# Optimization experiments

Measured on AMD Instinct MI355X. Metric: run time of the kernel, lower is better.

The kernel has to match this reference:

```python
import jax, jax.numpy as jnp
import numpy as np

SCALE = 100.0
ALPHA_MEM = 0.9
ALPHA_P = 0.99
ALPHA_MEM_OUT = 0.9

@jax.custom_vjp
def spike(x):
    return (x > 0).astype(x.dtype)

def _spike_fwd(x):
    return spike(x), x

def _spike_bwd(x, g):
    return (g / (SCALE * jnp.abs(x) + 1.0) ** 2,)

spike.defvjp(_spike_fwd, _spike_bwd)

B, T, N_IN, N, N_OUT = 64, 200, 128, 2048, 20

def setup_inputs() -> dict:
    key = jax.random.key(0)
    ks = jax.random.split(key, 6)
    inputs = jax.random.normal(ks[0], (B, T, N_IN), dtype=jnp.float32)
    w = jax.random.normal(ks[1], (N, N), dtype=jnp.float32) / np.sqrt(N)
    wscale_in = 1.0 - ALPHA_MEM
    w_in = jax.random.normal(ks[2], (N_IN, N), dtype=jnp.float32) * (wscale_in / np.sqrt(N_IN))
    wscale_out = 1.0 - ALPHA_MEM_OUT
    w_out = jax.random.normal(ks[3], (N, N_OUT), dtype=jnp.float32) * (wscale_out / np.sqrt(N))
    w_signs = jnp.sign(jax.random.normal(ks[4], (N,), dtype=jnp.float32))
    p = 0.1 * jax.random.normal(ks[5], (N,), dtype=jnp.float32)
    return {"inputs": inputs, "w": w, "w_in": w_in, "w_out": w_out,
            "w_signs": w_signs, "p": p}

def reference(inputs, w, w_in, w_out, w_signs, p):
    dt = inputs.dtype
    h1 = jnp.einsum('btc,cn->btn', inputs, w_in)          # [B,T,N]
    rec_w = w_signs[:, None] * jnp.abs(w)                  # [N,N]
    depr = (p < 0).astype(dt)                              # [N]

    def step(carry, h1_t):
        mem, w_p = carry
        mthr = mem - 1.0
        out = spike(mthr)
        rst = jax.lax.stop_gradient((mthr > 0).astype(dt))
        syn_p = jnp.einsum('bn,no->bo', out * (1.0 + w_p), rec_w)
        w_p_new = w_p * ALPHA_P + out * p * (1.0 + depr * w_p)
        mem_new = ALPHA_MEM * mem + h1_t + syn_p - rst
        return (mem_new, w_p_new), out

    zeros = jnp.zeros((h1.shape[0], rec_w.shape[0]), dtype=dt)
    _, spk = jax.lax.scan(step, (zeros, zeros), jnp.swapaxes(h1, 0, 1))
    spk_rec = jnp.swapaxes(spk, 0, 1)                      # [B,T,N]

    h2 = jnp.einsum('btn,no->bto', spk_rec, w_out)         # [B,T,O]

    def out_step(o, h2_t):
        o2 = ALPHA_MEM_OUT * o + h2_t
        return o2, o2

    o0 = jnp.zeros((h2.shape[0], h2.shape[2]), dtype=dt)
    _, outs = jax.lax.scan(out_step, o0, jnp.swapaxes(h2, 0, 1))
    return jnp.swapaxes(outs, 0, 1)                        # [B,T,O]
```

## Files before the change

kernel.cpp:

```cpp
#include <hip/hip_runtime.h>

#define BB   64
#define TT   200
#define NIN  128
#define NN   2048
#define NOUT 20

#define S    8
#define NWIN 25
#define ACAP 64
#define BCAP 128

typedef __attribute__((ext_vector_type(8))) short short8;
typedef __attribute__((ext_vector_type(4))) float f32x4;
typedef __attribute__((ext_vector_type(4))) _Float16 h16x4;

__device__ __forceinline__ void bf16split(float x, ushort& h, ushort& l) {
    unsigned u = __float_as_uint(x);
    unsigned hb = (u + 0x7FFFu + ((u >> 16) & 1u)) >> 16;
    h = (ushort)hb;
    float xh = __uint_as_float(hb << 16);
    float xl = x - xh;
    unsigned v = __float_as_uint(xl);
    l = (ushort)((v + 0x7FFFu + ((v >> 16) & 1u)) >> 16);
}

__global__ __launch_bounds__(256) void repack_a(
    const float* __restrict__ X, ushort* __restrict__ Ap)
{
    const int blk  = blockIdx.x;
    const int tid  = threadIdx.x;
    const int kc   = tid >> 6;
    const int lane = tid & 63;
    const int lr   = lane & 15, lg = lane >> 4;

    const float* src = X + (size_t)(blk * 16 + lr) * NIN + kc * 32 + lg * 8;
    float f[8];
    *(float4*)(f)     = *(const float4*)(src);
    *(float4*)(f + 4) = *(const float4*)(src + 4);

    short8 hv, lv;
    #pragma unroll
    for (int j = 0; j < 8; ++j) {
        ushort h, l;
        bf16split(f[j], h, l);
        hv[j] = (short)h; lv[j] = (short)l;
    }
    ushort* dst = Ap + (size_t)(blk * 4 + kc) * 1024 + lane * 8;
    *(short8*)(dst)       = hv;
    *(short8*)(dst + 512) = lv;
}

__global__ __launch_bounds__(256) void repack_b(
    const float* __restrict__ W, ushort* __restrict__ Bp)
{
    const int blk  = blockIdx.x;
    const int tid  = threadIdx.x;
    const int kc   = tid >> 6;
    const int lane = tid & 63;
    const int lr   = lane & 15, lg = lane >> 4;

    const float* src = W + (size_t)(kc * 32 + lg * 8) * NN + blk * 16 + lr;
    float f[8];
    #pragma unroll
    for (int j = 0; j < 8; ++j) f[j] = src[(size_t)j * NN];

    short8 hv, lv;
    #pragma unroll
    for (int j = 0; j < 8; ++j) {
        ushort h, l;
        bf16split(f[j], h, l);
        hv[j] = (short)h; lv[j] = (short)l;
    }
    ushort* dst = Bp + (size_t)(blk * 4 + kc) * 1024 + lane * 8;
    *(short8*)(dst)       = hv;
    *(short8*)(dst + 512) = lv;
}

__global__ __launch_bounds__(256, 2) void h1_mfma(
    const ushort* __restrict__ Ap, const ushort* __restrict__ Bp,
    _Float16* __restrict__ C)
{
    __shared__ ushort sbuf[2][16][1024];

    const int l   = blockIdx.y * gridDim.x + blockIdx.x;
    const int nl  = (l & 7) * 200 + (l >> 3);
    const int bx  = nl & 15, by = nl >> 4;

    const int tid  = threadIdx.x;
    const int w_   = tid >> 6, lane = tid & 63;
    const int lr   = lane & 15, lg = lane >> 4;
    const int m0   = by * 128, n0 = bx * 128;
    const int wr   = (w_ >> 1) * 64, wc = (w_ & 1) * 64;

    const ushort* pAs = Ap + (size_t)(m0 >> 4) * 4096;
    const ushort* pBs = Bp + (size_t)(n0 >> 4) * 4096;

#define STAGE(kc, nb)                                                        \
    do {                                                                     \
        _Pragma("unroll")                                                    \
        for (int i_ = 0; i_ < 8; ++i_) {                                     \
            const int idx_   = w_ * 8 + i_;                                  \
            const int side_  = idx_ >> 4;                                    \
            const int chunk_ = (idx_ >> 1) & 7;                              \
            const int hl_    = idx_ & 1;                                     \
            const ushort* g_ = (side_ ? pBs : pAs) + chunk_ * 4096           \
                               + (kc) * 1024 + hl_ * 512 + lane * 8;         \
            ushort* d_ = &sbuf[nb][idx_ >> 1][hl_ * 512];                    \
            __builtin_amdgcn_global_load_lds(                                \
                (const __attribute__((address_space(1))) void*)g_,           \
                (__attribute__((address_space(3))) void*)d_, 16, 0, 0);      \
        }                                                                    \
    } while (0)

    f32x4 acc[4][4];
    const f32x4 z = {0.f, 0.f, 0.f, 0.f};
    #pragma unroll
    for (int rb = 0; rb < 4; ++rb)
        #pragma unroll
        for (int cb = 0; cb < 4; ++cb) acc[rb][cb] = z;

    STAGE(0, 0);
    __syncthreads();

    const int ar = wr >> 4;
    const int br = 8 + (wc >> 4);

    #pragma unroll
    for (int kc = 0; kc < 4; ++kc) {
        const int cb_ = kc & 1;
        if (kc < 3) STAGE(kc + 1, cb_ ^ 1);

        short8 fah[4], fal[4], fbh[4], fbl[4];
        #pragma unroll
        for (int rb = 0; rb < 4; ++rb) {
            fah[rb] = *(const short8*)(&sbuf[cb_][ar + rb][lane * 8]);
            fal[rb] = *(const short8*)(&sbuf[cb_][ar + rb][512 + lane * 8]);
        }
        #pragma unroll
        for (int cb = 0; cb < 4; ++cb) {
            fbh[cb] = *(const short8*)(&sbuf[cb_][br + cb][lane * 8]);
            fbl[cb] = *(const short8*)(&sbuf[cb_][br + cb][512 + lane * 8]);
        }
        #pragma unroll
        for (int rb = 0; rb < 4; ++rb)
            #pragma unroll
            for (int cb = 0; cb < 4; ++cb) {
                acc[rb][cb] = __builtin_amdgcn_mfma_f32_16x16x32_bf16(
                    fbh[cb], fah[rb], acc[rb][cb], 0, 0, 0);
                acc[rb][cb] = __builtin_amdgcn_mfma_f32_16x16x32_bf16(
                    fbl[cb], fah[rb], acc[rb][cb], 0, 0, 0);
                acc[rb][cb] = __builtin_amdgcn_mfma_f32_16x16x32_bf16(
                    fbh[cb], fal[rb], acc[rb][cb], 0, 0, 0);
            }
        if (kc < 3) __syncthreads();
    }
#undef STAGE

    #pragma unroll
    for (int rb = 0; rb < 4; ++rb) {
        _Float16* Crow = C + (size_t)(m0 + wr + rb * 16 + lr) * NN
                           + n0 + wc + lg * 4;
        #pragma unroll
        for (int cb = 0; cb < 4; ++cb) {
            h16x4 hv;
            hv[0] = (_Float16)acc[rb][cb][0];
            hv[1] = (_Float16)acc[rb][cb][1];
            hv[2] = (_Float16)acc[rb][cb][2];
            hv[3] = (_Float16)acc[rb][cb][3];
            *(h16x4*)(Crow + cb * 16) = hv;
        }
    }
}

__global__ __launch_bounds__(512) void snn_scan(
    const _Float16* __restrict__ h1, const float* __restrict__ w,
    const float* __restrict__ w_signs, const float* __restrict__ pvec,
    const float* __restrict__ w_out, float* __restrict__ out)
{
    const int b   = blockIdx.x;
    const int tid = threadIdx.x;
    const int n0  = tid << 2;

    __shared__ int   s_amask[2];
    __shared__ int   s_acnt[2][S];
    __shared__ int   s_aidx[2][S][ACAP];
    __shared__ float s_aval[2][S][ACAP];
    __shared__ int   s_bcnt[2];
    __shared__ int   s_bidx[2][BCAP];
    __shared__ float s_bval[2][BCAP];

    if (tid < 2) { s_amask[tid] = 0; s_bcnt[tid] = 0; }
    if (tid < 2 * S) ((int*)s_acnt)[tid] = 0;

    float4 mem = {0.f,0.f,0.f,0.f}, wp = {0.f,0.f,0.f,0.f};
    const float4 p4 = *(const float4*)(pvec + n0);
    const float4 sg = *(const float4*)(w_signs + n0);
    float4 depr;
    depr.x = (p4.x < 0.f) ? 1.f : 0.f;  depr.y = (p4.y < 0.f) ? 1.f : 0.f;
    depr.z = (p4.z < 0.f) ? 1.f : 0.f;  depr.w = (p4.w < 0.f) ? 1.f : 0.f;

    const float P99[S] = {1.0f, 0.99f, 0.9801f, 0.970299f, 0.96059601f,
                          0.9509900499f, 0.941480149401f, 0.93206534790699f};
    const float P99_8 = 0.9227446944279201f;

    const _Float16* hb = h1 + (size_t)b * TT * NN + n0;
    float* outb = out + (size_t)b * TT * NOUT + tid;
    float o2 = 0.f;

    h16x4 PA[S], PB[S];
    #pragma unroll
    for (int j = 0; j < S; ++j) PA[j] = *(const h16x4*)(hb + (size_t)j * NN);
    __syncthreads();

#define RAWBAR()                                              \
    do { asm volatile("s_waitcnt lgkmcnt(0)" ::: "memory");   \
         __builtin_amdgcn_s_barrier();                        \
         asm volatile("" ::: "memory"); } while (0)

#define CVT4(v) { (float)(v)[0], (float)(v)[1], (float)(v)[2], (float)(v)[3] }

    auto window = [&](h16x4 (&Pc)[S], h16x4 (&Pf)[S], int wnd) {
        const int p  = wnd & 1;
        const int t0 = wnd * S;
        const float4 memB = mem, wpB = wp;

        #pragma unroll
        for (int j = 0; j < S; ++j) {
            const float4 a = CVT4(Pc[j]);
            int tp = t0 + j + S; if (tp > TT - 1) tp = TT - 1;
            Pf[j] = *(const h16x4*)(hb + (size_t)tp * NN);

            const float mx = fmaxf(fmaxf(mem.x, mem.y), fmaxf(mem.z, mem.w));
            if (__builtin_expect(mx > 1.f, 0)) {
                const bool f0 = mem.x > 1.f, f1 = mem.y > 1.f,
                           f2 = mem.z > 1.f, f3 = mem.w > 1.f;
                atomicOr(&s_amask[p], 1 << j);
                if (f0) { int k = atomicAdd(&s_acnt[p][j], 1);
                          if (k < ACAP) { s_aidx[p][j][k] = n0;
                                          s_aval[p][j][k] = (1.f + wp.x * P99[j]) * sg.x; } }
                if (f1) { int k = atomicAdd(&s_acnt[p][j], 1);
                          if (k < ACAP) { s_aidx[p][j][k] = n0 + 1;
                                          s_aval[p][j][k] = (1.f + wp.y * P99[j]) * sg.y; } }
                if (f2) { int k = atomicAdd(&s_acnt[p][j], 1);
                          if (k < ACAP) { s_aidx[p][j][k] = n0 + 2;
                                          s_aval[p][j][k] = (1.f + wp.z * P99[j]) * sg.z; } }
                if (f3) { int k = atomicAdd(&s_acnt[p][j], 1);
                          if (k < ACAP) { s_aidx[p][j][k] = n0 + 3;
                                          s_aval[p][j][k] = (1.f + wp.w * P99[j]) * sg.w; } }
                mem.x = fmaf(0.9f, mem.x, a.x) - (f0 ? 1.f : 0.f);
                mem.y = fmaf(0.9f, mem.y, a.y) - (f1 ? 1.f : 0.f);
                mem.z = fmaf(0.9f, mem.z, a.z) - (f2 ? 1.f : 0.f);
                mem.w = fmaf(0.9f, mem.w, a.w) - (f3 ? 1.f : 0.f);
            } else {
                mem.x = fmaf(0.9f, mem.x, a.x);
                mem.y = fmaf(0.9f, mem.y, a.y);
                mem.z = fmaf(0.9f, mem.z, a.z);
                mem.w = fmaf(0.9f, mem.w, a.w);
            }
        }

        RAWBAR();
        const int mask = s_amask[p];

        if (__builtin_expect(mask == 0, 1)) {
            wp.x *= P99_8; wp.y *= P99_8; wp.z *= P99_8; wp.w *= P99_8;
            if (tid < NOUT) {
                #pragma unroll
                for (int j = 0; j < S; ++j) {
                    o2 = 0.9f * o2;
                    outb[(size_t)(t0 + j) * NOUT] = o2;
                }
            }
            return;
        }

        const int tstar = __ffs(mask) - 1;

        int cntS = s_acnt[p][tstar]; if (cntS > ACAP) cntS = ACAP;
        int   pidx[4];
        float pval[4];
        float4 wpre[4];
        #pragma unroll
        for (int m_ = 0; m_ < 4; ++m_) {
            if (m_ < cntS) {
                pidx[m_] = s_aidx[p][tstar][m_];
                pval[m_] = s_aval[p][tstar][m_];
                wpre[m_] = *(const float4*)(w + (size_t)pidx[m_] * NN + n0);
            }
        }

        mem = memB; wp = wpB;
        #pragma unroll
        for (int j = 0; j < S; ++j) {
            const float4 a = CVT4(Pc[j]);
            if (j < tstar) {
                mem.x = fmaf(0.9f, mem.x, a.x);
                mem.y = fmaf(0.9f, mem.y, a.y);
                mem.z = fmaf(0.9f, mem.z, a.z);
                mem.w = fmaf(0.9f, mem.w, a.w);
                wp.x *= 0.99f; wp.y *= 0.99f; wp.z *= 0.99f; wp.w *= 0.99f;
                if (tid < NOUT) { o2 = 0.9f * o2;
                                  outb[(size_t)(t0 + j) * NOUT] = o2; }
            } else if (j == tstar) {
                const bool f0 = mem.x > 1.f, f1 = mem.y > 1.f,
                           f2 = mem.z > 1.f, f3 = mem.w > 1.f;
                float4 syn = {0.f,0.f,0.f,0.f};
                #pragma unroll
                for (int m_ = 0; m_ < 4; ++m_) {
                    if (m_ < cntS) {
                        syn.x = fmaf(pval[m_], fabsf(wpre[m_].x), syn.x);
                        syn.y = fmaf(pval[m_], fabsf(wpre[m_].y), syn.y);
                        syn.z = fmaf(pval[m_], fabsf(wpre[m_].z), syn.z);
                        syn.w = fmaf(pval[m_], fabsf(wpre[m_].w), syn.w);
                    }
                }
                for (int m = 4; m < cntS; ++m) {
                    const int nm = s_aidx[p][tstar][m];
                    const float vm = s_aval[p][tstar][m];
                    const float4 wr = *(const float4*)(w + (size_t)nm * NN + n0);
                    syn.x = fmaf(vm, fabsf(wr.x), syn.x);
                    syn.y = fmaf(vm, fabsf(wr.y), syn.y);
                    syn.z = fmaf(vm, fabsf(wr.z), syn.z);
                    syn.w = fmaf(vm, fabsf(wr.w), syn.w);
                }
                if (tid < NOUT) {
                    float c = 0.f;
                    for (int m = 0; m < cntS; ++m)
                        c += w_out[(size_t)s_aidx[p][tstar][m] * NOUT + tid];
                    o2 = 0.9f * o2 + c;
                    outb[(size_t)(t0 + j) * NOUT] = o2;
                }
                mem.x = fmaf(0.9f, mem.x, a.x) + syn.x - (f0 ? 1.f : 0.f);
                mem.y = fmaf(0.9f, mem.y, a.y) + syn.y - (f1 ? 1.f : 0.f);
                mem.z = fmaf(0.9f, mem.z, a.z) + syn.z - (f2 ? 1.f : 0.f);
                mem.w = fmaf(0.9f, mem.w, a.w) + syn.w - (f3 ? 1.f : 0.f);
                wp.x = f0 ? 0.99f*wp.x + p4.x*(1.f + depr.x*wp.x) : 0.99f*wp.x;
                wp.y = f1 ? 0.99f*wp.y + p4.y*(1.f + depr.y*wp.y) : 0.99f*wp.y;
                wp.z = f2 ? 0.99f*wp.z + p4.z*(1.f + depr.z*wp.z) : 0.99f*wp.z;
                wp.w = f3 ? 0.99f*wp.w + p4.w*(1.f + depr.w*wp.w) : 0.99f*wp.w;
            } else {
                const int par = j & 1;
                const bool f0 = mem.x > 1.f, f1 = mem.y > 1.f,
                           f2 = mem.z > 1.f, f3 = mem.w > 1.f;
                if (f0 | f1 | f2 | f3) {
                    if (f0) { int k = atomicAdd(&s_bcnt[par], 1); if (k < BCAP) {
                              s_bidx[par][k] = n0;     s_bval[par][k] = (1.f + wp.x) * sg.x; } }
                    if (f1) { int k = atomicAdd(&s_bcnt[par], 1); if (k < BCAP) {
                              s_bidx[par][k] = n0 + 1; s_bval[par][k] = (1.f + wp.y) * sg.y; } }
                    if (f2) { int k = atomicAdd(&s_bcnt[par], 1); if (k < BCAP) {
                              s_bidx[par][k] = n0 + 2; s_bval[par][k] = (1.f + wp.z) * sg.z; } }
                    if (f3) { int k = atomicAdd(&s_bcnt[par], 1); if (k < BCAP) {
                              s_bidx[par][k] = n0 + 3; s_bval[par][k] = (1.f + wp.w) * sg.w; } }
                }
                RAWBAR();
                int cnt = s_bcnt[par]; if (cnt > BCAP) cnt = BCAP;
                float4 syn = {0.f,0.f,0.f,0.f};
                if (__builtin_expect(cnt != 0, 0)) {
                    for (int m = 0; m < cnt; ++m) {
                        const int nm = s_bidx[par][m];
                        const float vm = s_bval[par][m];
                        const float4 wr = *(const float4*)(w + (size_t)nm * NN + n0);
                        syn.x = fmaf(vm, fabsf(wr.x), syn.x);
                        syn.y = fmaf(vm, fabsf(wr.y), syn.y);
                        syn.z = fmaf(vm, fabsf(wr.z), syn.z);
                        syn.w = fmaf(vm, fabsf(wr.w), syn.w);
                    }
                }
                if (tid < NOUT) {
                    float c = 0.f;
                    for (int m = 0; m < cnt; ++m)
                        c += w_out[(size_t)s_bidx[par][m] * NOUT + tid];
                    o2 = 0.9f * o2 + c;
                    outb[(size_t)(t0 + j) * NOUT] = o2;
                }
                mem.x = fmaf(0.9f, mem.x, a.x) + syn.x - (f0 ? 1.f : 0.f);
                mem.y = fmaf(0.9f, mem.y, a.y) + syn.y - (f1 ? 1.f : 0.f);
                mem.z = fmaf(0.9f, mem.z, a.z) + syn.z - (f2 ? 1.f : 0.f);
                mem.w = fmaf(0.9f, mem.w, a.w) + syn.w - (f3 ? 1.f : 0.f);
                wp.x = f0 ? 0.99f*wp.x + p4.x*(1.f + depr.x*wp.x) : 0.99f*wp.x;
                wp.y = f1 ? 0.99f*wp.y + p4.y*(1.f + depr.y*wp.y) : 0.99f*wp.y;
                wp.z = f2 ? 0.99f*wp.z + p4.z*(1.f + depr.z*wp.z) : 0.99f*wp.z;
                wp.w = f3 ? 0.99f*wp.w + p4.w*(1.f + depr.w*wp.w) : 0.99f*wp.w;
                if (__builtin_expect(cnt != 0, 0)) {
                    RAWBAR();
                    if (tid == 0) s_bcnt[par] = 0;
                }
            }
        }
        RAWBAR();
        if (tid < S) s_acnt[p][tid] = 0;
        else if (tid == S) s_amask[p] = 0;
    };

    for (int wnd = 0; wnd < NWIN - 1; wnd += 2) {
        window(PA, PB, wnd);
        window(PB, PA, wnd + 1);
    }
    window(PA, PB, NWIN - 1);
#undef CVT4
#undef RAWBAR
}

extern "C" void kernel_launch(void* const* d_in, const int* in_sizes, int n_in,
                              void* d_out, int out_size, void* d_ws, size_t ws_size,
                              hipStream_t stream) {
    (void)in_sizes; (void)n_in; (void)out_size; (void)ws_size;
    const float* inputs  = (const float*)d_in[0];
    const float* w       = (const float*)d_in[1];
    const float* w_in    = (const float*)d_in[2];
    const float* w_out   = (const float*)d_in[3];
    const float* w_signs = (const float*)d_in[4];
    const float* p       = (const float*)d_in[5];
    float* out = (float*)d_out;

    const size_t H1B = (size_t)BB * TT * NN * 2;
    const size_t APB = (size_t)800 * 4096 * 2;

    _Float16* h1 = (_Float16*)d_ws;
    ushort*   Ap = (ushort*)((char*)d_ws + H1B);
    ushort*   Bp = (ushort*)((char*)d_ws + H1B + APB);

    repack_a<<<800, 256, 0, stream>>>(inputs, Ap);
    repack_b<<<128, 256, 0, stream>>>(w_in, Bp);

    dim3 gg(NN / 128, (BB * TT) / 128);
    h1_mfma<<<gg, 256, 0, stream>>>(Ap, Bp, h1);

    snn_scan<<<BB, 512, 0, stream>>>(h1, w, w_signs, p, w_out, out);
}
```

Before: 85.30 us.

## Fuse input GEMM and SNN scan into one kernel with per-panel readiness flags

Merges the h1 GEMM and the recurrent scan into a single launch. The first 64 blocks run the per-batch scan and the remaining blocks compute GEMM tiles. The input rows are reordered time-major so each 128-row GEMM panel covers two timesteps for all batches. Scan blocks spin on global per-panel counters before consuming h1, so the scan can overlap with the GEMM instead of waiting for the whole launch to finish. This depends on the scan blocks being co-resident with the GEMM blocks and on the atomics for visibility, and the polling and smaller GEMM tiles add overhead.

```diff
diff --git a/kernel.cpp b/kernel.cpp
--- a/kernel.cpp
+++ b/kernel.cpp
@@ -11,9 +11,13 @@
 #define ACAP 64
 #define BCAP 128
 
+#define HSTRIDE (64 * NN)
+
 typedef __attribute__((ext_vector_type(8))) short short8;
 typedef __attribute__((ext_vector_type(4))) float f32x4;
 typedef __attribute__((ext_vector_type(4))) _Float16 h16x4;
+
+__device__ int g_pcnt[100];
 
 __device__ __forceinline__ void bf16split(float x, ushort& h, ushort& l) {
     unsigned u = __float_as_uint(x);
@@ -28,13 +32,16 @@
 __global__ __launch_bounds__(256) void repack_a(
     const float* __restrict__ X, ushort* __restrict__ Ap)
 {
+    if (blockIdx.x == 0 && threadIdx.x < 100) g_pcnt[threadIdx.x] = 0;
     const int blk  = blockIdx.x;
     const int tid  = threadIdx.x;
     const int kc   = tid >> 6;
     const int lane = tid & 63;
     const int lr   = lane & 15, lg = lane >> 4;
 
-    const float* src = X + (size_t)(blk * 16 + lr) * NIN + kc * 32 + lg * 8;
+    const int r  = blk * 16 + lr;
+    const int bb = r & 63, tt = r >> 6;
+    const float* src = X + ((size_t)bb * TT + tt) * NIN + kc * 32 + lg * 8;
     float f[8];
     *(float4*)(f)     = *(const float4*)(src);
     *(float4*)(f + 4) = *(const float4*)(src + 4);
@@ -77,118 +84,137 @@
     *(short8*)(dst + 512) = lv;
 }
 
-__global__ __launch_bounds__(256, 2) void h1_mfma(
+__global__ __launch_bounds__(512) void fused_gemm_scan(
     const ushort* __restrict__ Ap, const ushort* __restrict__ Bp,
-    _Float16* __restrict__ C)
+    _Float16* __restrict__ h1, const float* __restrict__ w,
+    const float* __restrict__ w_signs, const float* __restrict__ pvec,
+    const float* __restrict__ w_out, float* __restrict__ out)
 {
-    __shared__ ushort sbuf[2][16][1024];
-
-    const int l   = blockIdx.y * gridDim.x + blockIdx.x;
-    const int nl  = (l & 7) * 200 + (l >> 3);
-    const int bx  = nl & 15, by = nl >> 4;
-
-    const int tid  = threadIdx.x;
-    const int w_   = tid >> 6, lane = tid & 63;
-    const int lr   = lane & 15, lg = lane >> 4;
-    const int m0   = by * 128, n0 = bx * 128;
-    const int wr   = (w_ >> 1) * 64, wc = (w_ & 1) * 64;
-
-    const ushort* pAs = Ap + (size_t)(m0 >> 4) * 4096;
-    const ushort* pBs = Bp + (size_t)(n0 >> 4) * 4096;
-
-#define STAGE(kc, nb)                                                        \
+    __shared__ char smem_raw[65536];
+
+    const int l   = blockIdx.x;
+    const int tid = threadIdx.x;
+
+    if (l >= 64) {
+        ushort (*sbuf)[16][1024] = (ushort (*)[16][1024])smem_raw;
+
+        const int g     = l - 64;
+        const int panel = g >> 4;
+        const int nb    = g & 15;
+        const int m0 = panel * 128, n0 = nb * 128;
+        const int w_ = tid >> 6, lane = tid & 63;
+        const int lr = lane & 15, lg = lane >> 4;
+        const int wr = (w_ >> 2) * 64, wc = (w_ & 3) * 32;
+
+        const ushort* pAs = Ap + (size_t)(m0 >> 4) * 4096;
+        const ushort* pBs = Bp + (size_t)(n0 >> 4) * 4096;
+
+#define STAGE(kc, nbuf)                                                      \
     do {                                                                     \
         _Pragma("unroll")                                                    \
-        for (int i_ = 0; i_ < 8; ++i_) {                                     \
-            const int idx_   = w_ * 8 + i_;                                  \
+        for (int i_ = 0; i_ < 4; ++i_) {                                     \
+            const int idx_   = w_ * 4 + i_;                                  \
             const int side_  = idx_ >> 4;                                    \
             const int chunk_ = (idx_ >> 1) & 7;                              \
             const int hl_    = idx_ & 1;                                     \
             const ushort* g_ = (side_ ? pBs : pAs) + chunk_ * 4096           \
                                + (kc) * 1024 + hl_ * 512 + lane * 8;         \
-            ushort* d_ = &sbuf[nb][idx_ >> 1][hl_ * 512];                    \
+            ushort* d_ = &sbuf[nbuf][idx_ >> 1][hl_ * 512];                  \
             __builtin_amdgcn_global_load_lds(                                \
                 (const __attribute__((address_space(1))) void*)g_,           \
                 (__attribute__((address_space(3))) void*)d_, 16, 0, 0);      \
         }                                                                    \
     } while (0)
 
-    f32x4 acc[4][4];
-    const f32x4 z = {0.f, 0.f, 0.f, 0.f};
-    #pragma unroll
-    for (int rb = 0; rb < 4; ++rb)
-        #pragma unroll
-        for (int cb = 0; cb < 4; ++cb) acc[rb][cb] = z;
-
-    STAGE(0, 0);
-    __syncthreads();
-
-    const int ar = wr >> 4;
-    const int br = 8 + (wc >> 4);
-
-    #pragma unroll
-    for (int kc = 0; kc < 4; ++kc) {
-        const int cb_ = kc & 1;
-        if (kc < 3) STAGE(kc + 1, cb_ ^ 1);
-
-        short8 fah[4], fal[4], fbh[4], fbl[4];
-        #pragma unroll
-        for (int rb = 0; rb < 4; ++rb) {
-            fah[rb] = *(const short8*)(&sbuf[cb_][ar + rb][lane * 8]);
-            fal[rb] = *(const short8*)(&sbuf[cb_][ar + rb][512 + lane * 8]);
-        }
-        #pragma unroll
-        for (int cb = 0; cb < 4; ++cb) {
-            fbh[cb] = *(const short8*)(&sbuf[cb_][br + cb][lane * 8]);
-            fbl[cb] = *(const short8*)(&sbuf[cb_][br + cb][512 + lane * 8]);
-        }
+        f32x4 acc[4][2];
+        const f32x4 z = {0.f, 0.f, 0.f, 0.f};
         #pragma unroll
         for (int rb = 0; rb < 4; ++rb)
             #pragma unroll
-            for (int cb = 0; cb < 4; ++cb) {
-                acc[rb][cb] = __builtin_amdgcn_mfma_f32_16x16x32_bf16(
-                    fbh[cb], fah[rb], acc[rb][cb], 0, 0, 0);
-                acc[rb][cb] = __builtin_amdgcn_mfma_f32_16x16x32_bf16(
-                    fbl[cb], fah[rb], acc[rb][cb], 0, 0, 0);
-                acc[rb][cb] = __builtin_amdgcn_mfma_f32_16x16x32_bf16(
-                    fbh[cb], fal[rb], acc[rb][cb], 0, 0, 0);
-            }
-        if (kc < 3) __syncthreads();
+            for (int cb = 0; cb < 2; ++cb) acc[rb][cb] = z;
+
+        STAGE(0, 0);
+        __syncthreads();
+
+        const int ar = (w_ >> 2) * 4;
+        const int br = 8 + (w_ & 3) * 2;
+
+        #pragma unroll
+        for (int kc = 0; kc < 4; ++kc) {
+            const int cb_ = kc & 1;
+            if (kc < 3) STAGE(kc + 1, cb_ ^ 1);
+
+            short8 fah[4], fal[4], fbh[2], fbl[2];
+            #pragma unroll
+            for (int rb = 0; rb < 4; ++rb) {
+                fah[rb] = *(const short8*)(&sbuf[cb_][ar + rb][lane * 8]);
+                fal[rb] = *(const short8*)(&sbuf[cb_][ar + rb][512 + lane * 8]);
+            }
+            #pragma unroll
+            for (int cb = 0; cb < 2; ++cb) {
+                fbh[cb] = *(const short8*)(&sbuf[cb_][br + cb][lane * 8]);
+                fbl[cb] = *(const short8*)(&sbuf[cb_][br + cb][512 + lane * 8]);
+            }
+            #pragma unroll
+            for (int rb = 0; rb < 4; ++rb)
+                #pragma unroll
+                for (int cb = 0; cb < 2; ++cb) {
+                    acc[rb][cb] = __builtin_amdgcn_mfma_f32_16x16x32_bf16(
+                        fbh[cb], fah[rb], acc[rb][cb], 0, 0, 0);
+                    acc[rb][cb] = __builtin_amdgcn_mfma_f32_16x16x32_bf16(
+                        fbl[cb], fah[rb], acc[rb][cb], 0, 0, 0);
+                    acc[rb][cb] = __builtin_amdgcn_mfma_f32_16x16x32_bf16(
+                        fbh[cb], fal[rb], acc[rb][cb], 0, 0, 0);
+                }
+            if (kc < 3) __syncthreads();
+        }
+#undef STAGE
+
+        #pragma unroll
+        for (int rb = 0; rb < 4; ++rb) {
+            _Float16* Crow = h1 + (size_t)(m0 + wr + rb * 16 + lr) * NN
+                               + n0 + wc + lg * 4;
+            #pragma unroll
+            for (int cb = 0; cb < 2; ++cb) {
+                h16x4 hv;
+                hv[0] = (_Float16)acc[rb][cb][0];
+                hv[1] = (_Float16)acc[rb][cb][1];
+                hv[2] = (_Float16)acc[rb][cb][2];
+                hv[3] = (_Float16)acc[rb][cb][3];
+                unsigned long long uv;
+                __builtin_memcpy(&uv, &hv, 8);
+                __hip_atomic_store((unsigned long long*)(Crow + cb * 16), uv,
+                                   __ATOMIC_RELAXED, __HIP_MEMORY_SCOPE_SYSTEM);
+            }
+        }
+
+        __syncthreads();
+        if (tid == 0)
+            __hip_atomic_fetch_add(&g_pcnt[panel], 1,
+                                   __ATOMIC_RELAXED, __HIP_MEMORY_SCOPE_AGENT);
+        return;
     }
-#undef STAGE
-
-    #pragma unroll
-    for (int rb = 0; rb < 4; ++rb) {
-        _Float16* Crow = C + (size_t)(m0 + wr + rb * 16 + lr) * NN
-                           + n0 + wc + lg * 4;
-        #pragma unroll
-        for (int cb = 0; cb < 4; ++cb) {
-            h16x4 hv;
-            hv[0] = (_Float16)acc[rb][cb][0];
-            hv[1] = (_Float16)acc[rb][cb][1];
-            hv[2] = (_Float16)acc[rb][cb][2];
-            hv[3] = (_Float16)acc[rb][cb][3];
-            *(h16x4*)(Crow + cb * 16) = hv;
-        }
-    }
-}
-
-__global__ __launch_bounds__(512) void snn_scan(
-    const _Float16* __restrict__ h1, const float* __restrict__ w,
-    const float* __restrict__ w_signs, const float* __restrict__ pvec,
-    const float* __restrict__ w_out, float* __restrict__ out)
-{
-    const int b   = blockIdx.x;
-    const int tid = threadIdx.x;
-    const int n0  = tid << 2;
-
-    __shared__ int   s_amask[2];
-    __shared__ int   s_acnt[2][S];
-    __shared__ int   s_aidx[2][S][ACAP];
-    __shared__ float s_aval[2][S][ACAP];
-    __shared__ int   s_bcnt[2];
-    __shared__ int   s_bidx[2][BCAP];
-    __shared__ float s_bval[2][BCAP];
+
+    struct ScanShared {
+        int   amask[2];
+        int   acnt[2][S];
+        int   aidx[2][S][ACAP];
+        float aval[2][S][ACAP];
+        int   bcnt[2];
+        int   bidx[2][BCAP];
+        float bval[2][BCAP];
+    };
+    ScanShared* sp = (ScanShared*)smem_raw;
+    auto& s_amask = sp->amask;
+    auto& s_acnt  = sp->acnt;
+    auto& s_aidx  = sp->aidx;
+    auto& s_aval  = sp->aval;
+    auto& s_bcnt  = sp->bcnt;
+    auto& s_bidx  = sp->bidx;
+    auto& s_bval  = sp->bval;
+
+    const int b  = l;
+    const int n0 = tid << 2;
 
     if (tid < 2) { s_amask[tid] = 0; s_bcnt[tid] = 0; }
     if (tid < 2 * S) ((int*)s_acnt)[tid] = 0;
@@ -204,13 +230,29 @@
                           0.9509900499f, 0.941480149401f, 0.93206534790699f};
     const float P99_8 = 0.9227446944279201f;
 
-    const _Float16* hb = h1 + (size_t)b * TT * NN + n0;
+    const _Float16* hb = h1 + (size_t)b * NN + n0;
     float* outb = out + (size_t)b * TT * NOUT + tid;
     float o2 = 0.f;
+    int pdone = 0;
+
+#define POLLUP(P)                                                             \
+    do { if (tid == 0) {                                                      \
+            while (pdone <= (P)) {                                            \
+                int it_ = 0;                                                  \
+                while (__hip_atomic_load(&g_pcnt[pdone], __ATOMIC_RELAXED,    \
+                           __HIP_MEMORY_SCOPE_AGENT) < 16) {                  \
+                    __builtin_amdgcn_s_sleep(8);                              \
+                    if (++it_ > (1 << 22)) break; }                           \
+                ++pdone; }                                                    \
+         }                                                                    \
+         __syncthreads(); } while (0)
+
+    POLLUP(3);
 
     h16x4 PA[S], PB[S];
     #pragma unroll
-    for (int j = 0; j < S; ++j) PA[j] = *(const h16x4*)(hb + (size_t)j * NN);
+    for (int j = 0; j < S; ++j)
+        PA[j] = *(const h16x4*)(hb + (size_t)j * HSTRIDE);
     __syncthreads();
 
 #define RAWBAR()                                              \
@@ -225,11 +267,16 @@
         const int t0 = wnd * S;
         const float4 memB = mem, wpB = wp;
 
+        if (wnd < NWIN - 1) {
+            int pp = 4 * wnd + 7; if (pp > 99) pp = 99;
+            POLLUP(pp);
+        }
+
         #pragma unroll
         for (int j = 0; j < S; ++j) {
             const float4 a = CVT4(Pc[j]);
             int tp = t0 + j + S; if (tp > TT - 1) tp = TT - 1;
-            Pf[j] = *(const h16x4*)(hb + (size_t)tp * NN);
+            Pf[j] = *(const h16x4*)(hb + (size_t)tp * HSTRIDE);
 
             const float mx = fmaxf(fmaxf(mem.x, mem.y), fmaxf(mem.z, mem.w));
             if (__builtin_expect(mx > 1.f, 0)) {
@@ -400,6 +447,7 @@
     window(PA, PB, NWIN - 1);
 #undef CVT4
 #undef RAWBAR
+#undef POLLUP
 }
 
 extern "C" void kernel_launch(void* const* d_in, const int* in_sizes, int n_in,
@@ -424,8 +472,6 @@
     repack_a<<<800, 256, 0, stream>>>(inputs, Ap);
     repack_b<<<128, 256, 0, stream>>>(w_in, Bp);
 
-    dim3 gg(NN / 128, (BB * TT) / 128);
-    h1_mfma<<<gg, 256, 0, stream>>>(Ap, Bp, h1);
-
-    snn_scan<<<BB, 512, 0, stream>>>(h1, w, w_signs, p, w_out, out);
+    fused_gemm_scan<<<1664, 512, 0, stream>>>(Ap, Bp, h1, w, w_signs, p,
+                                              w_out, out);
 }
```

Result: slower. 111.4 us (+30.6%).
